# Kernel tuning notes

Measured on AMD Instinct MI355X. Metric: run time of the kernel, lower is better.

Reference implementation:

```python
import jax, jax.numpy as jnp
import numpy as np

LOCAL_K = 3
TOKEN_T, TOKEN_H, TOKEN_W = 8, 32, 32  # N = T*H*W = 8192
HIDDEN, N_HEADS = 256, 8


def _gather_neighbors(kv):
    # kv: [B, N, D2] -> [B, N, 27, D2] of 3x3x3 neighborhood (zero padded)
    B, N, D2 = kv.shape
    pad = LOCAL_K // 2
    x3d = kv.reshape(B, TOKEN_T, TOKEN_H, TOKEN_W, D2)
    x3d = jnp.pad(x3d, ((0, 0), (pad, pad), (pad, pad), (pad, pad), (0, 0)))
    slices = [
        x3d[:, dt:dt + TOKEN_T, dh:dh + TOKEN_H, dw:dw + TOKEN_W, :]
        for dt in range(LOCAL_K)
        for dh in range(LOCAL_K)
        for dw in range(LOCAL_K)
    ]
    nb = jnp.stack(slices, axis=4)  # [B, T, H, W, 27, D2]
    return nb.reshape(B, N, LOCAL_K ** 3, D2)


def setup_inputs() -> dict:
    key = jax.random.key(0)
    k1, k2, k3 = jax.random.split(key, 3)
    B, N, D = 2, TOKEN_T * TOKEN_H * TOKEN_W, HIDDEN
    x = jax.random.normal(k1, (B, N, D), dtype=jnp.float32)
    w_qkv = jax.random.normal(k2, (3 * D, D), dtype=jnp.float32) * (D ** -0.5)
    w_out = jax.random.normal(k3, (D, D), dtype=jnp.float32) * (D ** -0.5)
    return {"x": x, "w_qkv": w_qkv, "w_out": w_out}


def reference(x, w_qkv, w_out):
    B, N, D = x.shape
    H, d = N_HEADS, D // N_HEADS
    qkv = x @ w_qkv.T                       # [B, N, 3D]
    q, k, v = jnp.split(qkv, 3, axis=-1)
    kv_nb = _gather_neighbors(jnp.concatenate([k, v], axis=-1))  # [B,N,27,2D]
    k_nb, v_nb = jnp.split(kv_nb, 2, axis=-1)
    q = q.reshape(B, N, H, d)
    k_nb = k_nb.reshape(B, N, 27, H, d)
    v_nb = v_nb.reshape(B, N, 27, H, d)
    scale = 1.0 / jnp.sqrt(jnp.asarray(d, dtype=q.dtype))
    scores = jnp.einsum('bnhd,bnkhd->bnhk', q, k_nb) * scale  # [B,N,H,27]
    attn = jax.nn.softmax(scores, axis=-1)
    out = jnp.einsum('bnhk,bnkhd->bnhd', attn, v_nb)           # [B,N,H,d]
    return out.reshape(B, N, D) @ w_out.T
```

## Files before the change

kernel.cpp:

```cpp
#include <hip/hip_runtime.h>
#include <hip/hip_bf16.h>

#define TOK_T 8
#define TOK_H 32
#define TOK_W 32
#define NTOK 8192
#define BATCH 2
#define DMODEL 256
#define D3 768
#define NHEADS 8
#define DHEAD 32

using short8  = __attribute__((ext_vector_type(8))) short;
using ushort8 = __attribute__((ext_vector_type(8))) unsigned short;
using f32x4   = __attribute__((ext_vector_type(4))) float;

__device__ __forceinline__ ushort f2bf(float f) {
  union { float f; unsigned u; } v; v.f = f;
  unsigned u = v.u;
  unsigned r = (u + 0x7FFFu + ((u >> 16) & 1u)) >> 16;
  return (ushort)r;
}
__device__ __forceinline__ float bf2f(ushort u) {
  union { unsigned u; float f; } v; v.u = ((unsigned)u) << 16;
  return v.f;
}

template<int TBM, int TBN, int NW, bool AF32, bool OUTBF16>
__global__ __launch_bounds__(NW * 64, 4) void gemm_fused(const void* __restrict__ Av,
                                                         const float* __restrict__ B,
                                                         void* __restrict__ Cv,
                                                         int ldc) {
  constexpr int NCW = TBN / 64;
  constexpr int NWR = NW / NCW;
  constexpr int MR  = TBM / (NWR * 16);
  constexpr int CHA = TBM * 4;
  constexpr int CHB = TBN * 4;
  constexpr int NT  = NW * 64;
  constexpr int CPT = (CHA + CHB) / NT;
  constexpr int SA  = CHA / NT;
  constexpr int ATILE = TBM * 32;
  constexpr int BTILE = TBN * 32;

  __shared__ __align__(16) ushort sm[2][ATILE + BTILE];

  const int tid  = threadIdx.x;
  const int lane = tid & 63;
  const int wid  = tid >> 6;
  const int wr   = wid / NCW;
  const int wc   = wid % NCW;
  const int bm   = blockIdx.x * TBM;
  const int bn   = blockIdx.y * TBN;
  const int fr   = lane & 15;
  const int kb   = lane >> 4;

  f32x4 acc[MR][4] = {};
  float4  laf[SA > 0 ? SA : 1][2];
  ushort8 lab[SA > 0 ? SA : 1];
  float4  lbf[CPT - SA][2];

  auto load = [&](int kt) {
#pragma unroll
    for (int s = 0; s < SA; ++s) {
      int cc = tid + s * NT;
      int r = cc >> 2, sl = cc & 3;
      if constexpr (AF32) {
        const float* p = (const float*)Av + (size_t)(bm + r) * 256 + kt + sl * 8;
        laf[s][0] = *(const float4*)p;
        laf[s][1] = *(const float4*)(p + 4);
      } else {
        lab[s] = *(const ushort8*)((const ushort*)Av + (size_t)(bm + r) * 256 + kt + sl * 8);
      }
    }
#pragma unroll
    for (int s = 0; s < CPT - SA; ++s) {
      int cc = tid + (s + SA) * NT - CHA;
      int r = cc >> 2, sl = cc & 3;
      const float* p = B + (size_t)(bn + r) * 256 + kt + sl * 8;
      lbf[s][0] = *(const float4*)p;
      lbf[s][1] = *(const float4*)(p + 4);
    }
  };
  auto stow = [&](int buf) {
#pragma unroll
    for (int s = 0; s < SA; ++s) {
      int cc = tid + s * NT;
      int r = cc >> 2, sl = cc & 3;
      int sck = r * 4 + (sl ^ ((r >> 1) & 3));
      ushort8 v;
      if constexpr (AF32) {
        v[0] = f2bf(laf[s][0].x); v[1] = f2bf(laf[s][0].y);
        v[2] = f2bf(laf[s][0].z); v[3] = f2bf(laf[s][0].w);
        v[4] = f2bf(laf[s][1].x); v[5] = f2bf(laf[s][1].y);
        v[6] = f2bf(laf[s][1].z); v[7] = f2bf(laf[s][1].w);
      } else v = lab[s];
      *(ushort8*)&sm[buf][sck * 8] = v;
    }
#pragma unroll
    for (int s = 0; s < CPT - SA; ++s) {
      int cc = tid + (s + SA) * NT - CHA;
      int r = cc >> 2, sl = cc & 3;
      int sck = r * 4 + (sl ^ ((r >> 1) & 3));
      ushort8 v;
      v[0] = f2bf(lbf[s][0].x); v[1] = f2bf(lbf[s][0].y);
      v[2] = f2bf(lbf[s][0].z); v[3] = f2bf(lbf[s][0].w);
      v[4] = f2bf(lbf[s][1].x); v[5] = f2bf(lbf[s][1].y);
      v[6] = f2bf(lbf[s][1].z); v[7] = f2bf(lbf[s][1].w);
      *(ushort8*)&sm[buf][ATILE + sck * 8] = v;
    }
  };

  load(0);
  stow(0);
  __syncthreads();

  for (int it = 0; it < 8; ++it) {
    const int cur = it & 1;
    if (it < 7) load((it + 1) * 32);

    short8 af[MR], bf8[4];
#pragma unroll
    for (int m = 0; m < MR; ++m) {
      int r  = wr * (MR * 16) + m * 16 + fr;
      int ck = r * 4 + (kb ^ ((r >> 1) & 3));
      af[m] = *(const short8*)&sm[cur][ck * 8];
    }
#pragma unroll
    for (int n = 0; n < 4; ++n) {
      int r  = wc * 64 + n * 16 + fr;
      int ck = r * 4 + (kb ^ ((r >> 1) & 3));
      bf8[n] = *(const short8*)&sm[cur][ATILE + ck * 8];
    }
#pragma unroll
    for (int m = 0; m < MR; ++m)
#pragma unroll
      for (int n = 0; n < 4; ++n)
        acc[m][n] = __builtin_amdgcn_mfma_f32_16x16x32_bf16(af[m], bf8[n], acc[m][n], 0, 0, 0);

    if (it < 7) {
      stow(cur ^ 1);
      __syncthreads();
    }
  }

  if constexpr (OUTBF16) {
    ushort* C = (ushort*)Cv;
#pragma unroll
    for (int m = 0; m < MR; ++m)
#pragma unroll
      for (int n = 0; n < 4; ++n)
#pragma unroll
        for (int j = 0; j < 4; ++j) {
          int row = bm + wr * (MR * 16) + m * 16 + kb * 4 + j;
          int col = bn + wc * 64 + n * 16 + fr;
          C[(size_t)row * ldc + col] = f2bf(acc[m][n][j]);
        }
  } else {
    float* C = (float*)Cv;
#pragma unroll
    for (int m = 0; m < MR; ++m)
#pragma unroll
      for (int n = 0; n < 4; ++n)
#pragma unroll
        for (int j = 0; j < 4; ++j) {
          int row = bm + wr * (MR * 16) + m * 16 + kb * 4 + j;
          int col = bn + wc * 64 + n * 16 + fr;
          C[(size_t)row * ldc + col] = acc[m][n][j];
        }
  }
}

#define HALO 1000

__global__ __launch_bounds__(512, 2) void local_attn(const ushort* __restrict__ qkv,
                                                     ushort* __restrict__ aob) {
  __shared__ __align__(16) ushort sh[HALO * 64];
  const int ty   = blockIdx.x & 3;
  const int tx   = blockIdx.x >> 2;
  const int head = blockIdx.y;
  const int b    = blockIdx.z;
  const int h0 = ty * 8, w0 = tx * 8;
  const int tid = threadIdx.x;

  for (int idx = tid; idx < HALO; idx += 512) {
    int ht  = idx / 100;
    int rem = idx - ht * 100;
    int hh  = rem / 10;
    int hw  = rem - hh * 10;
    int gt = ht - 1, gh = h0 - 1 + hh, gw = w0 - 1 + hw;
    ushort* row = &sh[idx * 64];
    const int sw = idx & 7;
    if (gt >= 0 && gt < TOK_T && gh >= 0 && gh < TOK_H && gw >= 0 && gw < TOK_W) {
      size_t base = ((size_t)b * NTOK + (size_t)gt * 1024 + gh * 32 + gw) * D3;
      const ushort8* ks = (const ushort8*)(qkv + base + DMODEL + head * DHEAD);
      const ushort8* vs = (const ushort8*)(qkv + base + 2 * DMODEL + head * DHEAD);
#pragma unroll
      for (int p = 0; p < 4; ++p) *(ushort8*)&row[(p ^ sw) * 8]       = ks[p];
#pragma unroll
      for (int p = 0; p < 4; ++p) *(ushort8*)&row[((4 + p) ^ sw) * 8] = vs[p];
    } else {
      ushort8 z = (ushort8)0;
#pragma unroll
      for (int s = 0; s < 8; ++s) *(ushort8*)&row[s * 8] = z;
    }
  }

  const int tt = tid >> 6;
  const int th = (tid >> 3) & 7;
  const int tw = tid & 7;
  const int n  = tt * 1024 + (h0 + th) * 32 + (w0 + tw);

  const ushort* qp = qkv + ((size_t)b * NTOK + n) * D3 + head * DHEAD;
  float q[DHEAD];
  {
    const ushort8* qs = (const ushort8*)qp;
#pragma unroll
    for (int p = 0; p < 4; ++p) {
      ushort8 v = qs[p];
#pragma unroll
      for (int e = 0; e < 8; ++e) q[p * 8 + e] = bf2f(v[e]);
    }
  }
  __syncthreads();

  const float scale = 0.1767766952966369f;
  float s[27];
#pragma unroll
  for (int nb = 0; nb < 27; ++nb) {
    int dt = nb / 9, dh = (nb / 3) % 3, dw = nb % 3;
    int hidx = (tt + dt) * 100 + (th + dh) * 10 + (tw + dw);
    const ushort* row = &sh[hidx * 64];
    const int sw = hidx & 7;
    float a = 0.f;
#pragma unroll
    for (int p = 0; p < 4; ++p) {
      ushort8 kk = *(const ushort8*)&row[(p ^ sw) * 8];
#pragma unroll
      for (int e = 0; e < 8; ++e) a += q[p * 8 + e] * bf2f(kk[e]);
    }
    s[nb] = a * scale;
  }

  float mx = s[0];
#pragma unroll
  for (int nb = 1; nb < 27; ++nb) mx = fmaxf(mx, s[nb]);

  float o[DHEAD] = {};
  float sum = 0.f;
#pragma unroll
  for (int nb = 0; nb < 27; ++nb) {
    int dt = nb / 9, dh = (nb / 3) % 3, dw = nb % 3;
    int hidx = (tt + dt) * 100 + (th + dh) * 10 + (tw + dw);
    const ushort* row = &sh[hidx * 64];
    const int sw = hidx & 7;
    float p = __expf(s[nb] - mx);
    sum += p;
#pragma unroll
    for (int c = 0; c < 4; ++c) {
      ushort8 vv = *(const ushort8*)&row[((4 + c) ^ sw) * 8];
#pragma unroll
      for (int e = 0; e < 8; ++e) o[c * 8 + e] += p * bf2f(vv[e]);
    }
  }

  float inv = 1.f / sum;
  ushort8 os[4];
#pragma unroll
  for (int c = 0; c < 4; ++c)
#pragma unroll
    for (int e = 0; e < 8; ++e) os[c][e] = f2bf(o[c * 8 + e] * inv);
  ushort8* op = (ushort8*)(aob + ((size_t)b * NTOK + n) * DMODEL + head * DHEAD);
#pragma unroll
  for (int c = 0; c < 4; ++c) op[c] = os[c];
}

extern "C" void kernel_launch(void* const* d_in, const int* in_sizes, int n_in,
                              void* d_out, int out_size, void* d_ws, size_t ws_size,
                              hipStream_t stream) {
  const float* x     = (const float*)d_in[0];
  const float* w_qkv = (const float*)d_in[1];
  const float* w_out = (const float*)d_in[2];
  float* out = (float*)d_out;

  char* ws = (char*)d_ws;
  ushort* qkvb = (ushort*)ws;
  ushort* aob  = (ushort*)(ws + (size_t)BATCH * NTOK * D3 * 2);

  gemm_fused<128, 256, 8, true, true><<<dim3(128, 3), 512, 0, stream>>>(
      (const void*)x, w_qkv, (void*)qkvb, D3);

  local_attn<<<dim3(16, NHEADS, BATCH), 512, 0, stream>>>(qkvb, aob);

  gemm_fused<64, 128, 4, false, false><<<dim3(256, 2), 256, 0, stream>>>(
      (const void*)aob, w_out, (void*)out, DMODEL);
}
```

Before: 65.07 us.

## Split attention tiles along time, pack bf16 pairs for FMA, swap GEMM grid order

The local attention kernel now splits each 8x8 spatial tile into two 4-frame temporal halves. That doubles the block count to 512 with 256 threads each and uses a 600-row halo instead of 1000, so more blocks can be resident per CU. The inner dot-product and accumulation loops use packed float2 arithmetic with a cheap bf16-pair unpack, aiming at packed FMA instructions. The GEMM grids are transposed so that consecutive blocks share the same A rows, which should improve L2 reuse. The trade-off is more redundant halo loading, since the temporal overlap is now read twice.

```diff
diff --git a/kernel.cpp b/kernel.cpp
--- a/kernel.cpp
+++ b/kernel.cpp
@@ -14,6 +14,7 @@
 using short8  = __attribute__((ext_vector_type(8))) short;
 using ushort8 = __attribute__((ext_vector_type(8))) unsigned short;
 using f32x4   = __attribute__((ext_vector_type(4))) float;
+using f32x2   = __attribute__((ext_vector_type(2))) float;
 
 __device__ __forceinline__ ushort f2bf(float f) {
   union { float f; unsigned u; } v; v.f = f;
@@ -24,6 +25,13 @@
 __device__ __forceinline__ float bf2f(ushort u) {
   union { unsigned u; float f; } v; v.u = ((unsigned)u) << 16;
   return v.f;
+}
+__device__ __forceinline__ f32x2 bfpair(unsigned u) {
+  union { unsigned u; float f; } lo, hi;
+  lo.u = u << 16;
+  hi.u = u & 0xffff0000u;
+  f32x2 r; r[0] = lo.f; r[1] = hi.f;
+  return r;
 }
 
 template<int TBM, int TBN, int NW, bool AF32, bool OUTBF16>
@@ -49,8 +57,8 @@
   const int wid  = tid >> 6;
   const int wr   = wid / NCW;
   const int wc   = wid % NCW;
-  const int bm   = blockIdx.x * TBM;
-  const int bn   = blockIdx.y * TBN;
+  const int bm   = blockIdx.y * TBM;
+  const int bn   = blockIdx.x * TBN;
   const int fr   = lane & 15;
   const int kb   = lane >> 4;
 
@@ -170,24 +178,26 @@
   }
 }
 
-#define HALO 1000
-
-__global__ __launch_bounds__(512, 2) void local_attn(const ushort* __restrict__ qkv,
+#define HALO 600
+
+__global__ __launch_bounds__(256, 2) void local_attn(const ushort* __restrict__ qkv,
                                                      ushort* __restrict__ aob) {
   __shared__ __align__(16) ushort sh[HALO * 64];
-  const int ty   = blockIdx.x & 3;
-  const int tx   = blockIdx.x >> 2;
+  const int tile = blockIdx.x;
   const int head = blockIdx.y;
   const int b    = blockIdx.z;
-  const int h0 = ty * 8, w0 = tx * 8;
+  const int tz = tile >> 4;
+  const int ty = (tile >> 2) & 3;
+  const int tx = tile & 3;
+  const int t0 = tz * 4, h0 = ty * 8, w0 = tx * 8;
   const int tid = threadIdx.x;
 
-  for (int idx = tid; idx < HALO; idx += 512) {
+  for (int idx = tid; idx < HALO; idx += 256) {
     int ht  = idx / 100;
     int rem = idx - ht * 100;
     int hh  = rem / 10;
     int hw  = rem - hh * 10;
-    int gt = ht - 1, gh = h0 - 1 + hh, gw = w0 - 1 + hw;
+    int gt = t0 - 1 + ht, gh = h0 - 1 + hh, gw = w0 - 1 + hw;
     ushort* row = &sh[idx * 64];
     const int sw = idx & 7;
     if (gt >= 0 && gt < TOK_T && gh >= 0 && gh < TOK_H && gw >= 0 && gw < TOK_W) {
@@ -208,17 +218,19 @@
   const int tt = tid >> 6;
   const int th = (tid >> 3) & 7;
   const int tw = tid & 7;
-  const int n  = tt * 1024 + (h0 + th) * 32 + (w0 + tw);
+  const int n  = (t0 + tt) * 1024 + (h0 + th) * 32 + (w0 + tw);
 
   const ushort* qp = qkv + ((size_t)b * NTOK + n) * D3 + head * DHEAD;
-  float q[DHEAD];
+  f32x2 q2[16];
   {
     const ushort8* qs = (const ushort8*)qp;
 #pragma unroll
     for (int p = 0; p < 4; ++p) {
-      ushort8 v = qs[p];
-#pragma unroll
-      for (int e = 0; e < 8; ++e) q[p * 8 + e] = bf2f(v[e]);
+      union { ushort8 s; uint4 u; } v; v.s = qs[p];
+      q2[p * 4 + 0] = bfpair(v.u.x);
+      q2[p * 4 + 1] = bfpair(v.u.y);
+      q2[p * 4 + 2] = bfpair(v.u.z);
+      q2[p * 4 + 3] = bfpair(v.u.w);
     }
   }
   __syncthreads();
@@ -231,21 +243,23 @@
     int hidx = (tt + dt) * 100 + (th + dh) * 10 + (tw + dw);
     const ushort* row = &sh[hidx * 64];
     const int sw = hidx & 7;
-    float a = 0.f;
+    f32x2 a2 = {0.f, 0.f};
 #pragma unroll
     for (int p = 0; p < 4; ++p) {
-      ushort8 kk = *(const ushort8*)&row[(p ^ sw) * 8];
-#pragma unroll
-      for (int e = 0; e < 8; ++e) a += q[p * 8 + e] * bf2f(kk[e]);
-    }
-    s[nb] = a * scale;
+      union { ushort8 s; uint4 u; } kk; kk.s = *(const ushort8*)&row[(p ^ sw) * 8];
+      a2 += q2[p * 4 + 0] * bfpair(kk.u.x);
+      a2 += q2[p * 4 + 1] * bfpair(kk.u.y);
+      a2 += q2[p * 4 + 2] * bfpair(kk.u.z);
+      a2 += q2[p * 4 + 3] * bfpair(kk.u.w);
+    }
+    s[nb] = (a2[0] + a2[1]) * scale;
   }
 
   float mx = s[0];
 #pragma unroll
   for (int nb = 1; nb < 27; ++nb) mx = fmaxf(mx, s[nb]);
 
-  float o[DHEAD] = {};
+  f32x2 o2[16] = {};
   float sum = 0.f;
 #pragma unroll
   for (int nb = 0; nb < 27; ++nb) {
@@ -255,11 +269,14 @@
     const int sw = hidx & 7;
     float p = __expf(s[nb] - mx);
     sum += p;
+    f32x2 p2; p2[0] = p; p2[1] = p;
 #pragma unroll
     for (int c = 0; c < 4; ++c) {
-      ushort8 vv = *(const ushort8*)&row[((4 + c) ^ sw) * 8];
-#pragma unroll
-      for (int e = 0; e < 8; ++e) o[c * 8 + e] += p * bf2f(vv[e]);
+      union { ushort8 s; uint4 u; } vv; vv.s = *(const ushort8*)&row[((4 + c) ^ sw) * 8];
+      o2[c * 4 + 0] += p2 * bfpair(vv.u.x);
+      o2[c * 4 + 1] += p2 * bfpair(vv.u.y);
+      o2[c * 4 + 2] += p2 * bfpair(vv.u.z);
+      o2[c * 4 + 3] += p2 * bfpair(vv.u.w);
     }
   }
 
@@ -268,7 +285,8 @@
 #pragma unroll
   for (int c = 0; c < 4; ++c)
 #pragma unroll
-    for (int e = 0; e < 8; ++e) os[c][e] = f2bf(o[c * 8 + e] * inv);
+    for (int e = 0; e < 8; ++e)
+      os[c][e] = f2bf(o2[c * 4 + (e >> 1)][e & 1] * inv);
   ushort8* op = (ushort8*)(aob + ((size_t)b * NTOK + n) * DMODEL + head * DHEAD);
 #pragma unroll
   for (int c = 0; c < 4; ++c) op[c] = os[c];
@@ -286,11 +304,11 @@
   ushort* qkvb = (ushort*)ws;
   ushort* aob  = (ushort*)(ws + (size_t)BATCH * NTOK * D3 * 2);
 
-  gemm_fused<128, 256, 8, true, true><<<dim3(128, 3), 512, 0, stream>>>(
+  gemm_fused<128, 256, 8, true, true><<<dim3(3, 128), 512, 0, stream>>>(
       (const void*)x, w_qkv, (void*)qkvb, D3);
 
-  local_attn<<<dim3(16, NHEADS, BATCH), 512, 0, stream>>>(qkvb, aob);
-
-  gemm_fused<64, 128, 4, false, false><<<dim3(256, 2), 256, 0, stream>>>(
+  local_attn<<<dim3(32, NHEADS, BATCH), 256, 0, stream>>>(qkvb, aob);
+
+  gemm_fused<64, 128, 4, false, false><<<dim3(2, 256), 256, 0, stream>>>(
       (const void*)aob, w_out, (void*)out, DMODEL);
 }
```

Result: faster. 58.28 us (-10.4%).
